# Kernel optimization log

Measured on AMD Instinct MI355X. Metric: run time of the kernel, lower is better.

## Reference

```python
import jax, jax.numpy as jnp
import numpy as np

EMBED_DIM = 1024
NUM_HEADS = 16
HEAD_DIM = EMBED_DIM // NUM_HEADS
B, N = 4, 2048


def setup_inputs() -> dict:
    key = jax.random.key(0)
    k = jax.random.split(key, 5)
    scale = 1.0 / np.sqrt(EMBED_DIM)
    return {
        "x": jax.random.normal(k[0], (B, N, EMBED_DIM), dtype=jnp.float32),
        # torch nn.Linear convention: y = x @ W.T + b, W shape [out, in]
        "qkv_w": jax.random.uniform(k[1], (3 * EMBED_DIM, EMBED_DIM), jnp.float32, -scale, scale),
        "qkv_b": jax.random.uniform(k[2], (3 * EMBED_DIM,), jnp.float32, -scale, scale),
        "out_w": jax.random.uniform(k[3], (EMBED_DIM, EMBED_DIM), jnp.float32, -scale, scale),
        "out_b": jax.random.uniform(k[4], (EMBED_DIM,), jnp.float32, -scale, scale),
    }


def reference(x, qkv_w, qkv_b, out_w, out_b):
    b, n, e = x.shape
    qkv = x @ qkv_w.T + qkv_b                      # [B,N,3E]
    qkv = qkv.reshape(b, n, 3, NUM_HEADS, HEAD_DIM)
    qkv = jnp.transpose(qkv, (2, 0, 3, 1, 4))      # [3,B,H,N,D]
    q, k, v = qkv[0], qkv[1], qkv[2]
    scores = jnp.einsum("bhqd,bhkd->bhqk", q, k) / np.sqrt(HEAD_DIM)
    weights = jax.nn.softmax(scores, axis=-1)
    attn = jnp.einsum("bhqk,bhkd->bhqd", weights, v)  # [B,H,N,D]
    attn = jnp.transpose(attn, (0, 2, 1, 3)).reshape(b, n, e)
    return attn @ out_w.T + out_b
```

## Files before the change

kernel.cpp:

```cpp
#include <hip/hip_runtime.h>
#include <hip/hip_bf16.h>

#define EMBED 1024
#define NHEADS 16
#define HDIM 64
#define BATCH 4
#define SEQ 2048
#define MROWS (BATCH*SEQ)
#define QKVN (3*EMBED)
#define KDIM 1024

typedef __bf16 bf16;
typedef __bf16 bf16x4 __attribute__((ext_vector_type(4)));
typedef __bf16 bf16x8 __attribute__((ext_vector_type(8)));
typedef float f32x4 __attribute__((ext_vector_type(4)));
typedef float f32x16 __attribute__((ext_vector_type(16)));

#define QSCALE 0.18033688011112042f

#define SWB(B) ((B) ^ ((((B) >> 9) & 1) << 4) ^ ((((B) >> 7) & 1) << 5))

#define NX (MROWS*EMBED/4)
#define NQ (QKVN*KDIM/4)
#define NO (EMBED*KDIM/4)
__global__ void cvt_all(const float* __restrict__ x, const float* __restrict__ qw,
                        const float* __restrict__ ow,
                        bf16* __restrict__ xb, bf16* __restrict__ qwb, bf16* __restrict__ owb) {
    int i = blockIdx.x * blockDim.x + threadIdx.x;
    const float* src; bf16* dst; int j;
    if (i < NX)            { src = x;  dst = xb;  j = i; }
    else if (i < NX + NQ)  { src = qw; dst = qwb; j = i - NX; }
    else if (i < NX+NQ+NO) { src = ow; dst = owb; j = i - NX - NQ; }
    else return;
    float4 f = ((const float4*)src)[j];
    bf16x4 o;
    o[0] = (bf16)f.x; o[1] = (bf16)f.y; o[2] = (bf16)f.z; o[3] = (bf16)f.w;
    *((bf16x4*)dst + j) = o;
}

__launch_bounds__(256)
__global__ void gemm_qkv(const bf16* __restrict__ A, const bf16* __restrict__ B,
                         const float* __restrict__ bias,
                         bf16* __restrict__ Qb, bf16* __restrict__ Kb, bf16* __restrict__ Vt)
{
    __shared__ __align__(16) char ldsmem[32768];
    char* A0 = ldsmem;
    char* B0 = ldsmem + 8192;
    char* A1 = ldsmem + 16384;
    char* B1 = ldsmem + 24576;
    char* bnc = ldsmem;

    const int tid = threadIdx.x;
    const int l = tid & 63, w = tid >> 6;
    const int wr = w >> 1, wc = w & 1;
    const int lin = (blockIdx.x & 7) * 192 + (blockIdx.x >> 3);
    const int tM = (lin / 24) * 128, tN = (lin % 24) * 128;

    f32x4 acc[4][4] = {};
    const bf16* Abase = A + (size_t)tM * KDIM;
    const bf16* Bbase = B + (size_t)tN * KDIM;

#define GSTAGE(AL, BL, KOFF)                                                             \
    {                                                                                    \
        int koff_ = (KOFF) < KDIM ? (KOFF) : 0;                                          \
        _Pragma("unroll")                                                                \
        for (int t = 0; t < 2; ++t) {                                                    \
            int idx = t * 256 + tid;                                                     \
            int row = idx >> 2;                                                          \
            int kc = (idx & 3) * 8;                                                      \
            __builtin_amdgcn_global_load_lds(                                            \
                (const __attribute__((address_space(1))) void*)(Abase + (size_t)row * KDIM + koff_ + kc), \
                (__attribute__((address_space(3))) void*)((AL) + idx * 16), 16, 0, 0);   \
            __builtin_amdgcn_global_load_lds(                                            \
                (const __attribute__((address_space(1))) void*)(Bbase + (size_t)row * KDIM + koff_ + kc), \
                (__attribute__((address_space(3))) void*)((BL) + idx * 16), 16, 0, 0);   \
        }                                                                                \
    }

#define TBODY(CA, CB, NA, NB, KNEXT)                                                     \
    {                                                                                    \
        GSTAGE(NA, NB, KNEXT)                                                            \
        bf16x8 a[4], b[4];                                                               \
        _Pragma("unroll")                                                                \
        for (int i = 0; i < 4; ++i)                                                      \
            a[i] = *(const bf16x8*)((CA) + ((wr * 64 + i * 16 + (l & 15)) * 32 + (l >> 4) * 8) * 2); \
        _Pragma("unroll")                                                                \
        for (int j = 0; j < 4; ++j)                                                      \
            b[j] = *(const bf16x8*)((CB) + ((wc * 64 + j * 16 + (l & 15)) * 32 + (l >> 4) * 8) * 2); \
        asm volatile("s_waitcnt lgkmcnt(0)" ::: "memory");                               \
        __builtin_amdgcn_sched_barrier(0);                                               \
        __builtin_amdgcn_s_setprio(1);                                                   \
        _Pragma("unroll")                                                                \
        for (int i = 0; i < 4; ++i)                                                      \
            _Pragma("unroll")                                                            \
            for (int j = 0; j < 4; ++j)                                                  \
                acc[i][j] = __builtin_amdgcn_mfma_f32_16x16x32_bf16(a[i], b[j], acc[i][j], 0, 0, 0); \
        __builtin_amdgcn_s_setprio(0);                                                   \
        asm volatile("s_waitcnt vmcnt(0)" ::: "memory");                                 \
        __builtin_amdgcn_sched_barrier(0);                                               \
        __builtin_amdgcn_s_barrier();                                                    \
        __builtin_amdgcn_sched_barrier(0);                                               \
    }

    GSTAGE(A0, B0, 0)
    asm volatile("s_waitcnt vmcnt(0)" ::: "memory");
    __builtin_amdgcn_sched_barrier(0);
    __builtin_amdgcn_s_barrier();
    __builtin_amdgcn_sched_barrier(0);

    for (int k0 = 0; k0 < KDIM; k0 += 64) {
        TBODY(A0, B0, A1, B1, k0 + 32)
        TBODY(A1, B1, A0, B0, k0 + 64)
    }
#undef TBODY
#undef GSTAGE

    const int which = tN >> 10;
    const int bidx  = tM >> 11;
    const int hd0   = (tN & 1023) >> 6;
    const int t32base = (tM & 2047) >> 5;
    bf16* dstbase = (which == 0) ? Qb : (which == 1) ? Kb : Vt;
    const float scale = (which == 0) ? QSCALE : 1.0f;

    float bj[4];
    #pragma unroll
    for (int j = 0; j < 4; ++j)
        bj[j] = bias[tN + wc * 64 + j * 16 + (l & 15)];

    __syncthreads();
    #pragma unroll
    for (int i = 0; i < 4; ++i) {
        const int chunk_w = wc * 4 + wr * 2 + (i >> 1);
        #pragma unroll
        for (int j = 0; j < 4; ++j) {
            const int d = (wc * 64 + j * 16 + (l & 15)) & 63;
            #pragma unroll
            for (int r = 0; r < 4; ++r) {
                const int nsl = wr * 64 + i * 16 + (l >> 4) * 4 + r;
                float v = acc[i][j][r] + bj[j];
                int off;
                if (which == 2) {
                    int dblk = d >> 5;
                    int rem16 = nsl & 15;
                    int c = (nsl >> 4) & 1;
                    int fj = (rem16 & 3) | ((rem16 & 8) >> 1);
                    int fhi = (rem16 >> 2) & 1;
                    int lane = (d & 31) | (fhi << 5);
                    off = (dblk * 2 + c) * 512 + lane * 8 + fj;
                } else {
                    int kk = d >> 4, fhi = (d >> 3) & 1, fj = d & 7;
                    int lane = (nsl & 31) | (fhi << 5);
                    off = kk * 512 + lane * 8 + fj;
                }
                *(bf16*)(bnc + chunk_w * 4096 + SWB(off * 2)) = (bf16)(v * scale);
            }
        }
    }
    __syncthreads();
    #pragma unroll
    for (int cc = 0; cc < 2; ++cc) {
        const int c = (tid >> 6) + cc * 4;
        size_t gbase = ((size_t)(bidx * NHEADS + hd0 + (c >> 2)) * 64
                        + t32base + (c & 3)) * 2048;
        #pragma unroll
        for (int s = 0; s < 4; ++s) {
            int boff = SWB((s * 512 + (tid & 63) * 8) * 2);
            *(bf16x8*)(dstbase + gbase + (size_t)(s * 512 + (tid & 63) * 8)) =
                *(const bf16x8*)(bnc + c * 4096 + boff);
        }
    }
}

__launch_bounds__(256)
__global__ void gemm_out(const bf16* __restrict__ A, const bf16* __restrict__ B,
                         const float* __restrict__ bias, float* __restrict__ outF)
{
    __shared__ __align__(16) char lds64[24576];
    char* A0 = lds64;
    char* B0 = lds64 + 4096;
    char* A1 = lds64 + 12288;
    char* B1 = lds64 + 16384;
    const int tid = threadIdx.x;
    const int l = tid & 63, w = tid >> 6;
    const int lin = (blockIdx.x & 7) * 128 + (blockIdx.x >> 3);
    const int tM = (lin / 8) * 64, tN = (lin % 8) * 128;

    f32x4 acc[4][2] = {};
    const bf16* Abase = A + (size_t)tM * KDIM;
    const bf16* Bbase = B + (size_t)tN * KDIM;

#define OSTAGE(AL, BL, KOFF)                                                             \
    {                                                                                    \
        int koff_ = (KOFF) < KDIM ? (KOFF) : 0;                                          \
        {                                                                                \
            int row = tid >> 2;                                                          \
            int kc = (tid & 3) * 8;                                                      \
            __builtin_amdgcn_global_load_lds(                                            \
                (const __attribute__((address_space(1))) void*)(Abase + (size_t)row * KDIM + koff_ + kc), \
                (__attribute__((address_space(3))) void*)((AL) + tid * 16), 16, 0, 0);   \
        }                                                                                \
        _Pragma("unroll")                                                                \
        for (int t = 0; t < 2; ++t) {                                                    \
            int idx = t * 256 + tid;                                                     \
            int row = idx >> 2;                                                          \
            int kc = (idx & 3) * 8;                                                      \
            __builtin_amdgcn_global_load_lds(                                            \
                (const __attribute__((address_space(1))) void*)(Bbase + (size_t)row * KDIM + koff_ + kc), \
                (__attribute__((address_space(3))) void*)((BL) + idx * 16), 16, 0, 0);   \
        }                                                                                \
    }

#define OTBODY(CA, CB, NA, NB, KNEXT)                                                    \
    {                                                                                    \
        OSTAGE(NA, NB, KNEXT)                                                            \
        bf16x8 a[4], b[2];                                                               \
        _Pragma("unroll")                                                                \
        for (int i = 0; i < 4; ++i)                                                      \
            a[i] = *(const bf16x8*)((CA) + ((i * 16 + (l & 15)) * 32 + (l >> 4) * 8) * 2); \
        _Pragma("unroll")                                                                \
        for (int j = 0; j < 2; ++j)                                                      \
            b[j] = *(const bf16x8*)((CB) + ((w * 32 + j * 16 + (l & 15)) * 32 + (l >> 4) * 8) * 2); \
        asm volatile("s_waitcnt lgkmcnt(0)" ::: "memory");                               \
        __builtin_amdgcn_sched_barrier(0);                                               \
        __builtin_amdgcn_s_setprio(1);                                                   \
        _Pragma("unroll")                                                                \
        for (int i = 0; i < 4; ++i)                                                      \
            _Pragma("unroll")                                                            \
            for (int j = 0; j < 2; ++j)                                                  \
                acc[i][j] = __builtin_amdgcn_mfma_f32_16x16x32_bf16(a[i], b[j], acc[i][j], 0, 0, 0); \
        __builtin_amdgcn_s_setprio(0);                                                   \
        asm volatile("s_waitcnt vmcnt(0)" ::: "memory");                                 \
        __builtin_amdgcn_sched_barrier(0);                                               \
        __builtin_amdgcn_s_barrier();                                                    \
        __builtin_amdgcn_sched_barrier(0);                                               \
    }

    OSTAGE(A0, B0, 0)
    asm volatile("s_waitcnt vmcnt(0)" ::: "memory");
    __builtin_amdgcn_sched_barrier(0);
    __builtin_amdgcn_s_barrier();
    __builtin_amdgcn_sched_barrier(0);

    for (int k0 = 0; k0 < KDIM; k0 += 64) {
        OTBODY(A0, B0, A1, B1, k0 + 32)
        OTBODY(A1, B1, A0, B0, k0 + 64)
    }
#undef OTBODY
#undef OSTAGE

    #pragma unroll
    for (int i = 0; i < 4; ++i) {
        #pragma unroll
        for (int j = 0; j < 2; ++j) {
            int n = tN + w * 32 + j * 16 + (l & 15);
            float bv = bias[n];
            #pragma unroll
            for (int r = 0; r < 4; ++r) {
                int m = tM + i * 16 + (l >> 4) * 4 + r;
                outF[(size_t)m * EMBED + n] = acc[i][j][r] + bv;
            }
        }
    }
}

static __device__ __forceinline__ unsigned cvt_pk(float lo, float hi) {
    unsigned r;
    asm("v_cvt_pk_bf16_f32 %0, %1, %2" : "=v"(r) : "v"(lo), "v"(hi));
    return r;
}

__launch_bounds__(512)
__global__ void attn_kernel(const bf16* __restrict__ Qb, const bf16* __restrict__ Kb,
                            const bf16* __restrict__ Vt, bf16* __restrict__ AO)
{
    __shared__ bf16 kv[2][2][2048];
    const int tid = threadIdx.x, l = tid & 63, w = tid >> 6;
    const int lo5 = l & 31, hi = l >> 5;
    int bid = blockIdx.x;
    int swz = (bid & 7) * 64 + (bid >> 3);
    const int bh = swz >> 3;
    const int qt = swz & 7;

    const bf16* QFh = Qb + (size_t)bh * (64 * 2048);
    const bf16* srcp = ((w < 4) ? (Kb + (size_t)bh * (64 * 2048))
                                : (Vt + (size_t)bh * (64 * 2048)))
                       + (w & 3) * 512 + l * 8;

    const int qtile = qt * 8 + w;
    const bf16* qbase = QFh + (size_t)qtile * 2048 + (size_t)l * 8;
    bf16x8 qf[4];
    #pragma unroll
    for (int kk = 0; kk < 4; ++kk)
        qf[kk] = *(const bf16x8*)(qbase + kk * 512);

    f32x16 O0 = {}, O1 = {};
    float lsum = 0.f;

#define STAGE(BUF)                                                                       \
    {                                                                                    \
        __builtin_amdgcn_global_load_lds(                                                \
            (const __attribute__((address_space(1))) void*)srcp,                         \
            (__attribute__((address_space(3))) void*)&kv[BUF][w >> 2][(w & 3) * 512],    \
            16, 0, 0);                                                                   \
        srcp += 2048;                                                                    \
    }

    STAGE(0)
    __syncthreads();

#define ATTN_BODY(B)                                                                     \
    {                                                                                    \
        STAGE(B ^ 1)                                                                     \
        bf16x8 kK0 = *(const bf16x8*)&kv[B][0][0 * 512 + l * 8];                         \
        bf16x8 kK1 = *(const bf16x8*)&kv[B][0][1 * 512 + l * 8];                         \
        bf16x8 kK2 = *(const bf16x8*)&kv[B][0][2 * 512 + l * 8];                         \
        bf16x8 kK3 = *(const bf16x8*)&kv[B][0][3 * 512 + l * 8];                         \
        bf16x8 vf00 = *(const bf16x8*)&kv[B][1][0 * 512 + l * 8];                        \
        bf16x8 vf01 = *(const bf16x8*)&kv[B][1][1 * 512 + l * 8];                        \
        bf16x8 vf10 = *(const bf16x8*)&kv[B][1][2 * 512 + l * 8];                        \
        bf16x8 vf11 = *(const bf16x8*)&kv[B][1][3 * 512 + l * 8];                        \
        f32x16 S = {};                                                                   \
        __builtin_amdgcn_s_setprio(1);                                                   \
        S = __builtin_amdgcn_mfma_f32_32x32x16_bf16(kK0, qf[0], S, 0, 0, 0);             \
        S = __builtin_amdgcn_mfma_f32_32x32x16_bf16(kK1, qf[1], S, 0, 0, 0);             \
        S = __builtin_amdgcn_mfma_f32_32x32x16_bf16(kK2, qf[2], S, 0, 0, 0);             \
        S = __builtin_amdgcn_mfma_f32_32x32x16_bf16(kK3, qf[3], S, 0, 0, 0);             \
        __builtin_amdgcn_s_setprio(0);                                                   \
        float p[16];                                                                     \
        _Pragma("unroll")                                                                \
        for (int r = 0; r < 16; ++r)                                                     \
            p[r] = __builtin_amdgcn_exp2f(S[r]);                                         \
        float s0 = (p[0] + p[1]) + (p[2] + p[3]);                                        \
        float s1 = (p[4] + p[5]) + (p[6] + p[7]);                                        \
        float s2 = (p[8] + p[9]) + (p[10] + p[11]);                                      \
        float s3 = (p[12] + p[13]) + (p[14] + p[15]);                                    \
        lsum += (s0 + s1) + (s2 + s3);                                                   \
        union { unsigned u[4]; bf16x8 v; } pk0, pk1;                                     \
        pk0.u[0] = cvt_pk(p[0], p[1]);   pk0.u[1] = cvt_pk(p[2], p[3]);                  \
        pk0.u[2] = cvt_pk(p[4], p[5]);   pk0.u[3] = cvt_pk(p[6], p[7]);                  \
        pk1.u[0] = cvt_pk(p[8], p[9]);   pk1.u[1] = cvt_pk(p[10], p[11]);                \
        pk1.u[2] = cvt_pk(p[12], p[13]); pk1.u[3] = cvt_pk(p[14], p[15]);                \
        __builtin_amdgcn_s_setprio(1);                                                   \
        O0 = __builtin_amdgcn_mfma_f32_32x32x16_bf16(vf00, pk0.v, O0, 0, 0, 0);          \
        O0 = __builtin_amdgcn_mfma_f32_32x32x16_bf16(vf01, pk1.v, O0, 0, 0, 0);          \
        O1 = __builtin_amdgcn_mfma_f32_32x32x16_bf16(vf10, pk0.v, O1, 0, 0, 0);          \
        O1 = __builtin_amdgcn_mfma_f32_32x32x16_bf16(vf11, pk1.v, O1, 0, 0, 0);          \
        __builtin_amdgcn_s_setprio(0);                                                   \
        __syncthreads();                                                                 \
    }

    for (int t2 = 0; t2 < 64; t2 += 2) {
        ATTN_BODY(0)
        ATTN_BODY(1)
    }
#undef ATTN_BODY
#undef STAGE

    lsum += __shfl_xor(lsum, 32);
    float linv = 1.0f / lsum;

    const int b = bh >> 4, hd = bh & 15;
    const int q0 = qt * 256 + w * 32;
    bf16* outp = &AO[(size_t)(b * SEQ + q0 + lo5) * EMBED + hd * HDIM];
    #pragma unroll
    for (int g = 0; g < 4; ++g) {
        bf16x4 o0, o1;
        #pragma unroll
        for (int r4 = 0; r4 < 4; ++r4) {
            o0[r4] = (bf16)(O0[g * 4 + r4] * linv);
            o1[r4] = (bf16)(O1[g * 4 + r4] * linv);
        }
        *(bf16x4*)&outp[g * 8 + hi * 4] = o0;
        *(bf16x4*)&outp[32 + g * 8 + hi * 4] = o1;
    }
}

extern "C" void kernel_launch(void* const* d_in, const int* in_sizes, int n_in,
                              void* d_out, int out_size, void* d_ws, size_t ws_size,
                              hipStream_t stream) {
    const float* x     = (const float*)d_in[0];
    const float* qkv_w = (const float*)d_in[1];
    const float* qkv_b = (const float*)d_in[2];
    const float* out_w = (const float*)d_in[3];
    const float* out_b = (const float*)d_in[4];
    float* out = (float*)d_out;

    char* ws = (char*)d_ws;
    bf16* xb  = (bf16*)(ws);
    bf16* qwb = (bf16*)(ws + 16777216);
    bf16* owb = (bf16*)(ws + 23068672);
    bf16* Qb  = (bf16*)(ws + 25165824);
    bf16* Kb  = (bf16*)(ws + 41943040);
    bf16* Vt  = (bf16*)(ws + 58720256);
    bf16* AO  = (bf16*)(ws + 75497472);

    cvt_all<<<(NX + NQ + NO + 255) / 256, 256, 0, stream>>>(x, qkv_w, out_w, xb, qwb, owb);

    gemm_qkv<<<QKVN / 128 * (MROWS / 128), 256, 0, stream>>>(
        xb, qwb, qkv_b, Qb, Kb, Vt);

    attn_kernel<<<BATCH * NHEADS * (SEQ / 256), 512, 0, stream>>>(Qb, Kb, Vt, AO);

    gemm_out<<<EMBED / 128 * (MROWS / 64), 256, 0, stream>>>(AO, owb, out_b, out);
}
```

Measured before the change: 176.0 us.

## Process two query tiles per wave in attention to reuse staged K/V

Each wave now handles two 32-row query tiles, so each attention block covers 512 queries instead of 256 and the grid is halved. Every K/V tile staged into LDS is consumed by twice as many MFMA chains, which halves global K/V traffic and barrier count per query. The cost is doubled accumulator and Q-fragment registers, so launch bounds are pinned to one block per CU. With 256 blocks there is less parallelism and latency hiding, but more independent work per wave.

New measurement: 176.1 us. About the same (+0.1%).

```diff
diff --git a/kernel.cpp b/kernel.cpp
--- a/kernel.cpp
+++ b/kernel.cpp
@@ -269,7 +269,7 @@
     return r;
 }
 
-__launch_bounds__(512)
+__launch_bounds__(512, 1)
 __global__ void attn_kernel(const bf16* __restrict__ Qb, const bf16* __restrict__ Kb,
                             const bf16* __restrict__ Vt, bf16* __restrict__ AO)
 {
@@ -277,24 +277,28 @@
     const int tid = threadIdx.x, l = tid & 63, w = tid >> 6;
     const int lo5 = l & 31, hi = l >> 5;
     int bid = blockIdx.x;
-    int swz = (bid & 7) * 64 + (bid >> 3);
-    const int bh = swz >> 3;
-    const int qt = swz & 7;
+    int swz = (bid & 7) * 32 + (bid >> 3);
+    const int bh = swz >> 2;
+    const int qt = swz & 3;
 
     const bf16* QFh = Qb + (size_t)bh * (64 * 2048);
     const bf16* srcp = ((w < 4) ? (Kb + (size_t)bh * (64 * 2048))
                                 : (Vt + (size_t)bh * (64 * 2048)))
                        + (w & 3) * 512 + l * 8;
 
-    const int qtile = qt * 8 + w;
-    const bf16* qbase = QFh + (size_t)qtile * 2048 + (size_t)l * 8;
-    bf16x8 qf[4];
+    const int qtA = qt * 16 + 2 * w;
+    const int qtB = qtA + 1;
+    const bf16* qbaseA = QFh + (size_t)qtA * 2048 + (size_t)l * 8;
+    const bf16* qbaseB = QFh + (size_t)qtB * 2048 + (size_t)l * 8;
+    bf16x8 qfA[4], qfB[4];
     #pragma unroll
-    for (int kk = 0; kk < 4; ++kk)
-        qf[kk] = *(const bf16x8*)(qbase + kk * 512);
-
-    f32x16 O0 = {}, O1 = {};
-    float lsum = 0.f;
+    for (int kk = 0; kk < 4; ++kk) {
+        qfA[kk] = *(const bf16x8*)(qbaseA + kk * 512);
+        qfB[kk] = *(const bf16x8*)(qbaseB + kk * 512);
+    }
+
+    f32x16 OA0 = {}, OA1 = {}, OB0 = {}, OB1 = {};
+    float lsumA = 0.f, lsumB = 0.f;
 
 #define STAGE(BUF)                                                                       \
     {                                                                                    \
@@ -308,23 +312,14 @@
     STAGE(0)
     __syncthreads();
 
-#define ATTN_BODY(B)                                                                     \
-    {                                                                                    \
-        STAGE(B ^ 1)                                                                     \
-        bf16x8 kK0 = *(const bf16x8*)&kv[B][0][0 * 512 + l * 8];                         \
-        bf16x8 kK1 = *(const bf16x8*)&kv[B][0][1 * 512 + l * 8];                         \
-        bf16x8 kK2 = *(const bf16x8*)&kv[B][0][2 * 512 + l * 8];                         \
-        bf16x8 kK3 = *(const bf16x8*)&kv[B][0][3 * 512 + l * 8];                         \
-        bf16x8 vf00 = *(const bf16x8*)&kv[B][1][0 * 512 + l * 8];                        \
-        bf16x8 vf01 = *(const bf16x8*)&kv[B][1][1 * 512 + l * 8];                        \
-        bf16x8 vf10 = *(const bf16x8*)&kv[B][1][2 * 512 + l * 8];                        \
-        bf16x8 vf11 = *(const bf16x8*)&kv[B][1][3 * 512 + l * 8];                        \
+#define QHALF(QF, O0, O1, LSUM)                                                          \
+    {                                                                                    \
         f32x16 S = {};                                                                   \
         __builtin_amdgcn_s_setprio(1);                                                   \
-        S = __builtin_amdgcn_mfma_f32_32x32x16_bf16(kK0, qf[0], S, 0, 0, 0);             \
-        S = __builtin_amdgcn_mfma_f32_32x32x16_bf16(kK1, qf[1], S, 0, 0, 0);             \
-        S = __builtin_amdgcn_mfma_f32_32x32x16_bf16(kK2, qf[2], S, 0, 0, 0);             \
-        S = __builtin_amdgcn_mfma_f32_32x32x16_bf16(kK3, qf[3], S, 0, 0, 0);             \
+        S = __builtin_amdgcn_mfma_f32_32x32x16_bf16(kK0, QF[0], S, 0, 0, 0);             \
+        S = __builtin_amdgcn_mfma_f32_32x32x16_bf16(kK1, QF[1], S, 0, 0, 0);             \
+        S = __builtin_amdgcn_mfma_f32_32x32x16_bf16(kK2, QF[2], S, 0, 0, 0);             \
+        S = __builtin_amdgcn_mfma_f32_32x32x16_bf16(kK3, QF[3], S, 0, 0, 0);             \
         __builtin_amdgcn_s_setprio(0);                                                   \
         float p[16];                                                                     \
         _Pragma("unroll")                                                                \
@@ -334,7 +329,7 @@
         float s1 = (p[4] + p[5]) + (p[6] + p[7]);                                        \
         float s2 = (p[8] + p[9]) + (p[10] + p[11]);                                      \
         float s3 = (p[12] + p[13]) + (p[14] + p[15]);                                    \
-        lsum += (s0 + s1) + (s2 + s3);                                                   \
+        LSUM += (s0 + s1) + (s2 + s3);                                                   \
         union { unsigned u[4]; bf16x8 v; } pk0, pk1;                                     \
         pk0.u[0] = cvt_pk(p[0], p[1]);   pk0.u[1] = cvt_pk(p[2], p[3]);                  \
         pk0.u[2] = cvt_pk(p[4], p[5]);   pk0.u[3] = cvt_pk(p[6], p[7]);                  \
@@ -346,6 +341,21 @@
         O1 = __builtin_amdgcn_mfma_f32_32x32x16_bf16(vf10, pk0.v, O1, 0, 0, 0);          \
         O1 = __builtin_amdgcn_mfma_f32_32x32x16_bf16(vf11, pk1.v, O1, 0, 0, 0);          \
         __builtin_amdgcn_s_setprio(0);                                                   \
+    }
+
+#define ATTN_BODY(B)                                                                     \
+    {                                                                                    \
+        STAGE(B ^ 1)                                                                     \
+        bf16x8 kK0 = *(const bf16x8*)&kv[B][0][0 * 512 + l * 8];                         \
+        bf16x8 kK1 = *(const bf16x8*)&kv[B][0][1 * 512 + l * 8];                         \
+        bf16x8 kK2 = *(const bf16x8*)&kv[B][0][2 * 512 + l * 8];                         \
+        bf16x8 kK3 = *(const bf16x8*)&kv[B][0][3 * 512 + l * 8];                         \
+        bf16x8 vf00 = *(const bf16x8*)&kv[B][1][0 * 512 + l * 8];                        \
+        bf16x8 vf01 = *(const bf16x8*)&kv[B][1][1 * 512 + l * 8];                        \
+        bf16x8 vf10 = *(const bf16x8*)&kv[B][1][2 * 512 + l * 8];                        \
+        bf16x8 vf11 = *(const bf16x8*)&kv[B][1][3 * 512 + l * 8];                        \
+        QHALF(qfA, OA0, OA1, lsumA)                                                      \
+        QHALF(qfB, OB0, OB1, lsumB)                                                      \
         __syncthreads();                                                                 \
     }
 
@@ -354,24 +364,42 @@
         ATTN_BODY(1)
     }
 #undef ATTN_BODY
+#undef QHALF
 #undef STAGE
 
-    lsum += __shfl_xor(lsum, 32);
-    float linv = 1.0f / lsum;
+    lsumA += __shfl_xor(lsumA, 32);
+    lsumB += __shfl_xor(lsumB, 32);
+    float linvA = 1.0f / lsumA;
+    float linvB = 1.0f / lsumB;
 
     const int b = bh >> 4, hd = bh & 15;
-    const int q0 = qt * 256 + w * 32;
-    bf16* outp = &AO[(size_t)(b * SEQ + q0 + lo5) * EMBED + hd * HDIM];
-    #pragma unroll
-    for (int g = 0; g < 4; ++g) {
-        bf16x4 o0, o1;
+    {
+        bf16* outp = &AO[(size_t)(b * SEQ + qtA * 32 + lo5) * EMBED + hd * HDIM];
         #pragma unroll
-        for (int r4 = 0; r4 < 4; ++r4) {
-            o0[r4] = (bf16)(O0[g * 4 + r4] * linv);
-            o1[r4] = (bf16)(O1[g * 4 + r4] * linv);
+        for (int g = 0; g < 4; ++g) {
+            bf16x4 o0, o1;
+            #pragma unroll
+            for (int r4 = 0; r4 < 4; ++r4) {
+                o0[r4] = (bf16)(OA0[g * 4 + r4] * linvA);
+                o1[r4] = (bf16)(OA1[g * 4 + r4] * linvA);
+            }
+            *(bf16x4*)&outp[g * 8 + hi * 4] = o0;
+            *(bf16x4*)&outp[32 + g * 8 + hi * 4] = o1;
         }
-        *(bf16x4*)&outp[g * 8 + hi * 4] = o0;
-        *(bf16x4*)&outp[32 + g * 8 + hi * 4] = o1;
+    }
+    {
+        bf16* outp = &AO[(size_t)(b * SEQ + qtB * 32 + lo5) * EMBED + hd * HDIM];
+        #pragma unroll
+        for (int g = 0; g < 4; ++g) {
+            bf16x4 o0, o1;
+            #pragma unroll
+            for (int r4 = 0; r4 < 4; ++r4) {
+                o0[r4] = (bf16)(OB0[g * 4 + r4] * linvB);
+                o1[r4] = (bf16)(OB1[g * 4 + r4] * linvB);
+            }
+            *(bf16x4*)&outp[g * 8 + hi * 4] = o0;
+            *(bf16x4*)&outp[32 + g * 8 + hi * 4] = o1;
+        }
     }
 }
 
@@ -399,7 +427,7 @@
     gemm_qkv<<<QKVN / 128 * (MROWS / 128), 256, 0, stream>>>(
         xb, qwb, qkv_b, Qb, Kb, Vt);
 
-    attn_kernel<<<BATCH * NHEADS * (SEQ / 256), 512, 0, stream>>>(Qb, Kb, Vt, AO);
+    attn_kernel<<<BATCH * NHEADS * (SEQ / 512), 512, 0, stream>>>(Qb, Kb, Vt, AO);
 
     gemm_out<<<EMBED / 128 * (MROWS / 64), 256, 0, stream>>>(AO, owb, out_b, out);
 }
```
